# Kernel optimization log

Measured on AMD Instinct MI355X. Metric: run time of the kernel, lower is better.

Reference implementation:

```python
import jax, jax.numpy as jnp
import numpy as np

BLOCKS, LAYERS, KS = 4, 2, 2
DILATIONS = [2 ** i for _ in range(BLOCKS) for i in range(LAYERS)]  # [1,2]*4
B, C_IN, N, T = 16, 2, 2048, 12
RC, DC, SC, EC, OUT = 32, 32, 256, 512, 12
L = BLOCKS * LAYERS
BN_EPS = 1e-5


def setup_inputs() -> dict:
    key = jax.random.key(0)
    ks = jax.random.split(key, 24)
    # raw inputs
    x = jax.random.normal(ks[0], (B, C_IN, N, T), dtype=jnp.float32)
    # two fixed supports: row-normalized random adjacency (dense, as in GraphWaveNet transition matrices)
    A_raw = jax.random.uniform(ks[1], (2, N, N), dtype=jnp.float32)
    A = A_raw / jnp.sum(A_raw, axis=2, keepdims=True)
    nodevec1 = jax.random.normal(ks[2], (N, 10), dtype=jnp.float32)
    nodevec2 = jax.random.normal(ks[3], (10, N), dtype=jnp.float32)
    s = 0.1  # weight scale to keep activations in a sane range
    filter_w = jax.random.normal(ks[4], (L, DC, RC, KS), dtype=jnp.float32) * s
    filter_b = jax.random.normal(ks[5], (L, DC), dtype=jnp.float32) * s
    gate_w = jax.random.normal(ks[6], (L, DC, RC, KS), dtype=jnp.float32) * s
    gate_b = jax.random.normal(ks[7], (L, DC), dtype=jnp.float32) * s
    skip_w = jax.random.normal(ks[8], (L, SC, DC), dtype=jnp.float32) * s
    skip_b = jax.random.normal(ks[9], (L, SC), dtype=jnp.float32) * s
    gcn_w = jax.random.normal(ks[10], (L, RC, 7 * DC), dtype=jnp.float32) * s
    gcn_b = jax.random.normal(ks[11], (L, RC), dtype=jnp.float32) * s
    bn_gamma = 1.0 + 0.1 * jax.random.normal(ks[12], (L, RC), dtype=jnp.float32)
    bn_beta = 0.1 * jax.random.normal(ks[13], (L, RC), dtype=jnp.float32)
    bn_mean = 0.1 * jax.random.normal(ks[14], (L, RC), dtype=jnp.float32)
    bn_var = 1.0 + jax.random.uniform(ks[15], (L, RC), dtype=jnp.float32)
    start_w = jax.random.normal(ks[16], (RC, C_IN), dtype=jnp.float32) * s
    start_b = jax.random.normal(ks[17], (RC,), dtype=jnp.float32) * s
    end1_w = jax.random.normal(ks[18], (EC, SC), dtype=jnp.float32) * s
    end1_b = jax.random.normal(ks[19], (EC,), dtype=jnp.float32) * s
    end2_w = jax.random.normal(ks[20], (OUT, EC), dtype=jnp.float32) * s
    end2_b = jax.random.normal(ks[21], (OUT,), dtype=jnp.float32) * s
    return dict(x=x, A=A, nodevec1=nodevec1, nodevec2=nodevec2,
                filter_w=filter_w, filter_b=filter_b, gate_w=gate_w, gate_b=gate_b,
                skip_w=skip_w, skip_b=skip_b, gcn_w=gcn_w, gcn_b=gcn_b,
                bn_gamma=bn_gamma, bn_beta=bn_beta, bn_mean=bn_mean, bn_var=bn_var,
                start_w=start_w, start_b=start_b, end1_w=end1_w, end1_b=end1_b,
                end2_w=end2_w, end2_b=end2_b)


def _conv1x1(x, w, b):
    # x: [b,c,n,t], w: [o,c] -> [b,o,n,t]
    return jnp.einsum('oc,bcnt->bont', w, x) + b[None, :, None, None]


def _dilated_conv2(x, w, b, d):
    # kernel (1,2) with time dilation d; out length T-d (valid conv)
    xa, xb = x[..., :-d], x[..., d:]
    y = jnp.einsum('oc,bcnt->bont', w[:, :, 0], xa) + jnp.einsum('oc,bcnt->bont', w[:, :, 1], xb)
    return y + b[None, :, None, None]


def _fwd(x, A, nodevec1, nodevec2, filter_w, filter_b, gate_w, gate_b,
         skip_w, skip_b, gcn_w, gcn_b, bn_gamma, bn_beta, bn_mean, bn_var,
         start_w, start_b, end1_w, end1_b, end2_w, end2_b):
    # pad 1 step at the start of time; T becomes 13 == receptive_field
    x = jnp.pad(x, ((0, 0), (0, 0), (0, 0), (1, 0)))
    x = x[:, :2]
    x = _conv1x1(x, start_w, start_b)  # [B,RC,N,13]
    # adaptive adjacency
    adp = jax.nn.softmax(jax.nn.relu(nodevec1 @ nodevec2), axis=1)
    supports = [A[0], A[1], adp]
    skip = None
    for i, d in enumerate(DILATIONS):
        residual = x
        filt = jnp.tanh(_dilated_conv2(residual, filter_w[i], filter_b[i], d))
        gate = jax.nn.sigmoid(_dilated_conv2(residual, gate_w[i], gate_b[i], d))
        x = filt * gate  # [B,DC,N,T-d]
        s = _conv1x1(x, skip_w[i], skip_b[i])  # [B,SC,N,T']
        skip = s if skip is None else s + skip[..., -s.shape[3]:]
        # GCN: order-2 diffusion over 3 supports, concat, 1x1 mix (dropout is identity in eval)
        outs = [x]
        for a in supports:
            x1 = jnp.einsum('bcvt,vw->bcwt', x, a)
            x2 = jnp.einsum('bcvt,vw->bcwt', x1, a)
            outs.extend([x1, x2])
        h = jnp.concatenate(outs, axis=1)  # [B,7*DC,N,T']
        x = _conv1x1(h, gcn_w[i], gcn_b[i])
        x = x + residual[..., -x.shape[3]:]
        # BatchNorm2d in eval mode (running stats)
        inv = bn_gamma[i] / jnp.sqrt(bn_var[i] + BN_EPS)
        x = (x - bn_mean[i][None, :, None, None]) * inv[None, :, None, None] + bn_beta[i][None, :, None, None]
    x = jax.nn.relu(skip)
    x = jax.nn.relu(_conv1x1(x, end1_w, end1_b))
    x = _conv1x1(x, end2_w, end2_b)  # [B,OUT,N,1]
    return x


def reference(x, A, nodevec1, nodevec2, filter_w, filter_b, gate_w, gate_b,
              skip_w, skip_b, gcn_w, gcn_b, bn_gamma, bn_beta, bn_mean, bn_var,
              start_w, start_b, end1_w, end1_b, end2_w, end2_b):
    return _fwd(x, A, nodevec1, nodevec2, filter_w, filter_b, gate_w, gate_b,
                skip_w, skip_b, gcn_w, gcn_b, bn_gamma, bn_beta, bn_mean, bn_var,
                start_w, start_b, end1_w, end1_b, end2_w, end2_b)
```

## Files before the change

kernel.cpp:

```cpp
#include <hip/hip_runtime.h>
#include <math.h>


#define NNODE 2048
#define NLAYER 8
#define SSTR ((size_t)NNODE * NNODE)

typedef unsigned short u16;
typedef unsigned int u32;
typedef __attribute__((ext_vector_type(8))) short bf16x8;
typedef __attribute__((ext_vector_type(4))) float f32x4;

__device__ __forceinline__ u16 f2bf(float f) {
    unsigned u = __builtin_bit_cast(unsigned, f);
    u += 0x7fffu + ((u >> 16) & 1u);
    return (u16)(u >> 16);
}
__device__ __forceinline__ float bf2f(u16 h) {
    unsigned u = ((unsigned)h) << 16;
    return __builtin_bit_cast(float, u);
}
__device__ __forceinline__ float bflo(u32 p) { return __builtin_bit_cast(float, p << 16); }
__device__ __forceinline__ float bfhi(u32 p) { return __builtin_bit_cast(float, p & 0xffff0000u); }
__device__ __forceinline__ u32 pack2(float a, float b) {
    return (u32)f2bf(a) | ((u32)f2bf(b) << 16);
}

__device__ __forceinline__ void gld16(const void* g, void* l) {
    __builtin_amdgcn_global_load_lds(
        (const __attribute__((address_space(1))) unsigned int*)g,
        (__attribute__((address_space(3))) unsigned int*)l, 16, 0, 0);
}

__global__ __launch_bounds__(256) void k_adp_mm(const float* __restrict__ nv1,
                                                const float* __restrict__ nv2,
                                                float* __restrict__ P) {
    int v = blockIdx.y;
    int w = blockIdx.x * 256 + threadIdx.x;
    float acc = 0.f;
#pragma unroll
    for (int k = 0; k < 10; ++k) acc += nv1[v * 10 + k] * nv2[k * NNODE + w];
    P[(size_t)v * NNODE + w] = acc;
}

__global__ __launch_bounds__(256) void k_softmax(float* __restrict__ P) {
    int v = blockIdx.x, tid = threadIdx.x;
    float* row = P + (size_t)v * NNODE;
    float m = 0.f;
    for (int w = tid; w < NNODE; w += 256) m = fmaxf(m, fmaxf(row[w], 0.f));
#pragma unroll
    for (int off = 32; off > 0; off >>= 1) m = fmaxf(m, __shfl_down(m, off));
    __shared__ float redm[4];
    __shared__ float reds[4];
    int wave = tid >> 6, lane = tid & 63;
    if (lane == 0) redm[wave] = m;
    __syncthreads();
    m = fmaxf(fmaxf(redm[0], redm[1]), fmaxf(redm[2], redm[3]));
    float s = 0.f;
    for (int w = tid; w < NNODE; w += 256) s += expf(fmaxf(row[w], 0.f) - m);
#pragma unroll
    for (int off = 32; off > 0; off >>= 1) s += __shfl_down(s, off);
    if (lane == 0) reds[wave] = s;
    __syncthreads();
    s = reds[0] + reds[1] + reds[2] + reds[3];
    float inv = 1.f / s;
    for (int w = tid; w < NNODE; w += 256) row[w] = expf(fmaxf(row[w], 0.f) - m) * inv;
}

__global__ __launch_bounds__(256) void k_transp(const float* __restrict__ A,
                                                const float* __restrict__ adp,
                                                u16* __restrict__ ST,
                                                u16* __restrict__ Sbf) {
    __shared__ float tile[32][33];
    int s = blockIdx.z;
    const float* src = (s < 2) ? (A + (size_t)s * SSTR) : adp;
    int v0 = blockIdx.y * 32, w0 = blockIdx.x * 32;
    int tx = threadIdx.x & 31, ty = threadIdx.x >> 5;
    u16* dst2 = Sbf + (size_t)s * SSTR;
#pragma unroll
    for (int p = 0; p < 4; ++p) {
        float v = src[(size_t)(v0 + ty + p * 8) * NNODE + w0 + tx];
        tile[ty + p * 8][tx] = v;
        dst2[(size_t)(v0 + ty + p * 8) * NNODE + w0 + tx] = f2bf(v);
    }
    __syncthreads();
    u16* dst = ST + (size_t)(2 * s) * SSTR;
#pragma unroll
    for (int p = 0; p < 4; ++p)
        dst[(size_t)(w0 + ty + p * 8) * NNODE + v0 + tx] = f2bf(tile[tx][ty + p * 8]);
}

__global__ __launch_bounds__(256) void k_gemm_mfma(
    const u16* __restrict__ A, int lda, size_t asstr,
    const u16* __restrict__ BT, size_t bsstr,
    u16* __restrict__ C, int ldc, size_t csstr, int sbase) {
    __shared__ u16 Asl[128 * 32];
    __shared__ u16 Bsl[128 * 32];
    const int tid = threadIdx.x;
    const int wave = tid >> 6, lane = tid & 63;
    const int sidx = sbase + blockIdx.z;
    const u16* Ab = A + sidx * asstr + (size_t)blockIdx.y * 128 * lda;
    const u16* Bb = BT + sidx * bsstr + (size_t)blockIdx.x * 128 * NNODE;
    const int tr = tid >> 2;
    const int tc = (tid & 3) * 8;
    char* AslB = (char*)Asl + wave * 1024;
    char* BslB = (char*)Bsl + wave * 1024;
    const int wm = (wave & 1) * 64, wn = (wave >> 1) * 64;
    const int fr = lane & 15;
    const int fk = (lane >> 4) * 8;
    f32x4 acc[4][4];
#pragma unroll
    for (int i = 0; i < 4; ++i)
#pragma unroll
        for (int j = 0; j < 4; ++j) acc[i][j] = (f32x4){0.f, 0.f, 0.f, 0.f};

    for (int k0 = 0; k0 < 2048; k0 += 32) {
        gld16(Ab + (size_t)tr * lda + k0 + tc, AslB);
        gld16(Ab + (size_t)(tr + 64) * lda + k0 + tc, AslB + 4096);
        gld16(Bb + (size_t)tr * NNODE + k0 + tc, BslB);
        gld16(Bb + (size_t)(tr + 64) * NNODE + k0 + tc, BslB + 4096);
        __syncthreads();
        bf16x8 af[4], bf[4];
#pragma unroll
        for (int i = 0; i < 4; ++i)
            af[i] = *(const bf16x8*)&Asl[(wm + i * 16 + fr) * 32 + fk];
#pragma unroll
        for (int j = 0; j < 4; ++j)
            bf[j] = *(const bf16x8*)&Bsl[(wn + j * 16 + fr) * 32 + fk];
#pragma unroll
        for (int i = 0; i < 4; ++i)
#pragma unroll
            for (int j = 0; j < 4; ++j)
                acc[i][j] = __builtin_amdgcn_mfma_f32_16x16x32_bf16(af[i], bf[j], acc[i][j], 0, 0, 0);
        __syncthreads();
    }
    u16* Cb = C + sidx * csstr + (size_t)(blockIdx.y * 128 + wm) * ldc + blockIdx.x * 128 + wn;
    const int orow = (lane >> 4) * 4;
#pragma unroll
    for (int i = 0; i < 4; ++i)
#pragma unroll
        for (int j = 0; j < 4; ++j)
#pragma unroll
            for (int r = 0; r < 4; ++r)
                Cb[(size_t)(i * 16 + orow + r) * ldc + j * 16 + fr] = f2bf(acc[i][j][r]);
}

__global__ __launch_bounds__(256) void k_gemmZ(const u16* __restrict__ Xg,
                                               const u16* __restrict__ ST,
                                               u16* __restrict__ Z, int pass) {
    __shared__ u16 Asl[128 * 32];
    __shared__ u16 Bsl[128 * 32];
    const int tid = threadIdx.x;
    const int wave = tid >> 6, lane = tid & 63;
    const int m0 = blockIdx.x * 128;
    const int sl = blockIdx.y >> 4;
    const int nIn = (blockIdx.y & 15) * 128;
    const int slice = pass * 3 + sl;
    const u16* Ab = Xg + (size_t)m0 * 2048;
    const u16* Bb = ST + (size_t)slice * SSTR + (size_t)nIn * NNODE;
    const int tr = tid >> 2;
    const int tc = (tid & 3) * 8;
    char* AslB = (char*)Asl + wave * 1024;
    char* BslB = (char*)Bsl + wave * 1024;
    const int wm = (wave & 1) * 64, wn = (wave >> 1) * 64;
    const int fr = lane & 15;
    const int fk = (lane >> 4) * 8;
    f32x4 acc[4][4];
#pragma unroll
    for (int i = 0; i < 4; ++i)
#pragma unroll
        for (int j = 0; j < 4; ++j) acc[i][j] = (f32x4){0.f, 0.f, 0.f, 0.f};

    for (int k0 = 0; k0 < 2048; k0 += 32) {
        gld16(Ab + (size_t)tr * 2048 + k0 + tc, AslB);
        gld16(Ab + (size_t)(tr + 64) * 2048 + k0 + tc, AslB + 4096);
        gld16(Bb + (size_t)tr * NNODE + k0 + tc, BslB);
        gld16(Bb + (size_t)(tr + 64) * NNODE + k0 + tc, BslB + 4096);
        __syncthreads();
        bf16x8 af[4], bf[4];
#pragma unroll
        for (int i = 0; i < 4; ++i)
            af[i] = *(const bf16x8*)&Asl[(wm + i * 16 + fr) * 32 + fk];
#pragma unroll
        for (int j = 0; j < 4; ++j)
            bf[j] = *(const bf16x8*)&Bsl[(wn + j * 16 + fr) * 32 + fk];
#pragma unroll
        for (int i = 0; i < 4; ++i)
#pragma unroll
            for (int j = 0; j < 4; ++j)
                acc[i][j] = __builtin_amdgcn_mfma_f32_16x16x32_bf16(af[i], bf[j], acc[i][j], 0, 0, 0);
        __syncthreads();
    }
    u16* Cb = Z + (size_t)(m0 + wm) * 6144 + sl * 2048 + nIn + wn;
    const int orow = (lane >> 4) * 4;
#pragma unroll
    for (int i = 0; i < 4; ++i)
#pragma unroll
        for (int j = 0; j < 4; ++j)
#pragma unroll
            for (int r = 0; r < 4; ++r)
                Cb[(size_t)(i * 16 + orow + r) * 6144 + j * 16 + fr] = f2bf(acc[i][j][r]);
}

__global__ __launch_bounds__(256) void k_start(const float* __restrict__ xin,
                                               const float* __restrict__ sw,
                                               const float* __restrict__ sb,
                                               u16* __restrict__ out, int b0) {
    int n = blockIdx.x * 256 + threadIdx.x;
    int t = blockIdx.y;
    int bl = blockIdx.z;
    int b = b0 + bl;
    float x0 = 0.f, x1 = 0.f;
    if (t > 0) {
        x0 = xin[((size_t)(b * 2 + 0) * NNODE + n) * 12 + (t - 1)];
        x1 = xin[((size_t)(b * 2 + 1) * NNODE + n) * 12 + (t - 1)];
    }
#pragma unroll
    for (int co = 0; co < 32; ++co) {
        float v = sw[co * 2 + 0] * x0 + sw[co * 2 + 1] * x1 + sb[co];
        out[((size_t)(bl * 32 + co) * 13 + t) * NNODE + n] = f2bf(v);
    }
}

__global__ __launch_bounds__(256) void k_gate(const u16* __restrict__ cur,
                                              u16* __restrict__ xg,
                                              u16* __restrict__ nxt,
                                              int T, int Tn, int d,
                                              const float* __restrict__ fw,
                                              const float* __restrict__ fb,
                                              const float* __restrict__ gw,
                                              const float* __restrict__ gb,
                                              const float* __restrict__ gcwl,
                                              const float* __restrict__ gcbl,
                                              int donxt) {
    __shared__ float4 wp[1024];
    __shared__ float w0[32][33];
    int tid = threadIdx.x;
#pragma unroll
    for (int u = 0; u < 4; ++u) {
        int idx = tid + u * 256;
        int ci = idx >> 5, co = idx & 31;
        wp[idx] = make_float4(fw[co * 64 + ci * 2], fw[co * 64 + ci * 2 + 1],
                              gw[co * 64 + ci * 2], gw[co * 64 + ci * 2 + 1]);
        w0[ci][co] = gcwl[co * 224 + ci];
    }
    __syncthreads();
    int n = blockIdx.x * 512 + tid * 2;
    int t = blockIdx.y;
    int bl = blockIdx.z;
    float f0[32], f1[32], g0[32], g1[32];
#pragma unroll
    for (int co = 0; co < 32; ++co) { f0[co] = 0.f; f1[co] = 0.f; g0[co] = 0.f; g1[co] = 0.f; }
    for (int ci = 0; ci < 32; ++ci) {
        size_t ba = ((size_t)(bl * 32 + ci) * T + t) * NNODE + n;
        size_t bb = ((size_t)(bl * 32 + ci) * T + t + d) * NNODE + n;
        u32 ua = *(const u32*)&cur[ba];
        u32 ub = *(const u32*)&cur[bb];
        float xa0 = bflo(ua), xa1 = bfhi(ua);
        float xb0 = bflo(ub), xb1 = bfhi(ub);
#pragma unroll
        for (int co = 0; co < 32; ++co) {
            float4 w = wp[ci * 32 + co];
            f0[co] += w.x * xa0 + w.y * xb0;
            f1[co] += w.x * xa1 + w.y * xb1;
            g0[co] += w.z * xa0 + w.w * xb0;
            g1[co] += w.z * xa1 + w.w * xb1;
        }
    }
#pragma unroll
    for (int co = 0; co < 32; ++co) {
        float fbv = fb[co], gbv = gb[co];
        float a0 = tanhf(f0[co] + fbv) * (1.f / (1.f + expf(-(g0[co] + gbv))));
        float a1 = tanhf(f1[co] + fbv) * (1.f / (1.f + expf(-(g1[co] + gbv))));
        f0[co] = a0; f1[co] = a1;
        size_t o = ((size_t)(bl * 32 + co) * Tn + t) * NNODE + n;
        *(u32*)&xg[o] = pack2(a0, a1);
    }
    if (donxt) {
#pragma unroll
        for (int cop = 0; cop < 32; ++cop) {
            float s0 = gcbl[cop], s1 = s0;
#pragma unroll
            for (int ci = 0; ci < 32; ++ci) {
                float wv = w0[ci][cop];
                s0 += wv * f0[ci];
                s1 += wv * f1[ci];
            }
            size_t o = ((size_t)(bl * 32 + cop) * Tn + t) * NNODE + n;
            *(u32*)&nxt[o] = pack2(s0, s1);
        }
    }
}

__global__ __launch_bounds__(256) void k_skip(const u16* __restrict__ xg,
                                              float* __restrict__ skip, int Tn,
                                              const float* __restrict__ sw,
                                              const float* __restrict__ sb, int b0, int init) {
    __shared__ float wl[256];
    int tid = threadIdx.x;
    int sc0 = blockIdx.y * 8;
    wl[tid] = sw[sc0 * 32 + tid];
    __syncthreads();
    int n = blockIdx.x * 512 + tid * 2;
    int bl = blockIdx.z;
    float a0[8], a1[8];
#pragma unroll
    for (int j = 0; j < 8; ++j) { a0[j] = 0.f; a1[j] = 0.f; }
    for (int ci = 0; ci < 32; ci += 2) {
        u32 p0 = *(const u32*)&xg[((size_t)(bl * 32 + ci + 0) * Tn + (Tn - 1)) * NNODE + n];
        u32 p1 = *(const u32*)&xg[((size_t)(bl * 32 + ci + 1) * Tn + (Tn - 1)) * NNODE + n];
        float v00 = bflo(p0), v01 = bfhi(p0);
        float v10 = bflo(p1), v11 = bfhi(p1);
#pragma unroll
        for (int j = 0; j < 8; ++j) {
            float wA = wl[j * 32 + ci], wB = wl[j * 32 + ci + 1];
            a0[j] += wA * v00 + wB * v10;
            a1[j] += wA * v01 + wB * v11;
        }
    }
    int b = b0 + bl;
#pragma unroll
    for (int j = 0; j < 8; ++j) {
        size_t o = ((size_t)(b * 256) + sc0 + j) * NNODE + n;
        float bsv = sb[sc0 + j];
        if (init) {
            *(float2*)&skip[o] = make_float2(a0[j] + bsv, a1[j] + bsv);
        } else {
            float2 old = *(const float2*)&skip[o];
            *(float2*)&skip[o] = make_float2(old.x + a0[j] + bsv, old.y + a1[j] + bsv);
        }
    }
}

__global__ __launch_bounds__(256) void k_accum(const u16* __restrict__ Z,
                                               int cbase,
                                               const float* __restrict__ gcnw,
                                               u16* __restrict__ outp,
                                               const u16* __restrict__ resid,
                                               int Tn, int d, int finalf,
                                               const float* __restrict__ bng,
                                               const float* __restrict__ bnb,
                                               const float* __restrict__ bnm,
                                               const float* __restrict__ bnv) {
    __shared__ float wl[3][32][32];
    int tid = threadIdx.x;
    for (int u = tid; u < 3072; u += 256) {
        int g = u >> 10, ci = (u >> 5) & 31, co = u & 31;
        wl[g][ci][co] = gcnw[co * 224 + cbase + g * 32 + ci];
    }
    __syncthreads();
    int n = blockIdx.x * 512 + tid * 2;
    int t = blockIdx.y, bl = blockIdx.z;
    float a0[32], a1[32];
#pragma unroll
    for (int co = 0; co < 32; ++co) { a0[co] = 0.f; a1[co] = 0.f; }
    for (int ci = 0; ci < 32; ++ci) {
        size_t m = (size_t)(bl * 32 + ci) * Tn + t;
#pragma unroll
        for (int g = 0; g < 3; ++g) {
            u32 zz = *(const u32*)&Z[m * 6144 + g * 2048 + n];
            float v0 = bflo(zz), v1 = bfhi(zz);
#pragma unroll
            for (int cq = 0; cq < 8; ++cq) {
                float4 w = *(const float4*)&wl[g][ci][cq * 4];
                a0[cq * 4 + 0] += w.x * v0; a1[cq * 4 + 0] += w.x * v1;
                a0[cq * 4 + 1] += w.y * v0; a1[cq * 4 + 1] += w.y * v1;
                a0[cq * 4 + 2] += w.z * v0; a1[cq * 4 + 2] += w.z * v1;
                a0[cq * 4 + 3] += w.w * v0; a1[cq * 4 + 3] += w.w * v1;
            }
        }
    }
#pragma unroll
    for (int co = 0; co < 32; ++co) {
        size_t o = ((size_t)(bl * 32 + co) * Tn + t) * NNODE + n;
        u32 oo = *(const u32*)&outp[o];
        float v0 = bflo(oo) + a0[co];
        float v1 = bfhi(oo) + a1[co];
        if (finalf) {
            size_t ro = ((size_t)(bl * 32 + co) * (Tn + d) + t + d) * NNODE + n;
            u32 rr = *(const u32*)&resid[ro];
            v0 += bflo(rr); v1 += bfhi(rr);
            float inv = bng[co] * rsqrtf(bnv[co] + 1e-5f);
            float mu = bnm[co], be = bnb[co];
            v0 = (v0 - mu) * inv + be;
            v1 = (v1 - mu) * inv + be;
        }
        *(u32*)&outp[o] = pack2(v0, v1);
    }
}

__global__ __launch_bounds__(256) void k_skipT(const float* __restrict__ skip,
                                               u16* __restrict__ skipT) {
    __shared__ float tile[32][33];
    int b = blockIdx.z;
    int n0 = blockIdx.x * 32, c0 = blockIdx.y * 32;
    int tx = threadIdx.x & 31, ty = threadIdx.x >> 5;
#pragma unroll
    for (int p = 0; p < 4; ++p)
        tile[ty + p * 8][tx] = skip[((size_t)b * 256 + c0 + ty + p * 8) * NNODE + n0 + tx];
    __syncthreads();
#pragma unroll
    for (int p = 0; p < 4; ++p)
        skipT[((size_t)b * NNODE + n0 + ty + p * 8) * 256 + c0 + tx] =
            f2bf(fmaxf(tile[tx][ty + p * 8], 0.f));
}

__global__ __launch_bounds__(256) void k_cast(const float* __restrict__ src,
                                              u16* __restrict__ dst) {
    int i = blockIdx.x * 256 + threadIdx.x;
    dst[i] = f2bf(src[i]);
}

__global__ __launch_bounds__(256) void k_end1m(const u16* __restrict__ E1,
                                               const u16* __restrict__ skT,
                                               const float* __restrict__ bias,
                                               u16* __restrict__ h) {
    __shared__ u16 Asl[128 * 32];
    __shared__ u16 Bsl[128 * 32];
    const int tid = threadIdx.x;
    const int wave = tid >> 6, lane = tid & 63;
    const int b = blockIdx.z;
    const int m0 = blockIdx.y * 128;
    const int n0 = blockIdx.x * 128;
    const int tr = tid >> 2;
    const int tc = (tid & 3) * 8;
    char* AslB = (char*)Asl + wave * 1024;
    char* BslB = (char*)Bsl + wave * 1024;
    const int wm = (wave & 1) * 64, wn = (wave >> 1) * 64;
    const int fr = lane & 15;
    const int fk = (lane >> 4) * 8;
    const u16* Ab = E1 + (size_t)m0 * 256;
    const u16* Bb = skT + ((size_t)b * NNODE + n0) * 256;
    f32x4 acc[4][4];
#pragma unroll
    for (int i = 0; i < 4; ++i)
#pragma unroll
        for (int j = 0; j < 4; ++j) acc[i][j] = (f32x4){0.f, 0.f, 0.f, 0.f};
    for (int k0 = 0; k0 < 256; k0 += 32) {
        gld16(Ab + (size_t)tr * 256 + k0 + tc, AslB);
        gld16(Ab + (size_t)(tr + 64) * 256 + k0 + tc, AslB + 4096);
        gld16(Bb + (size_t)tr * 256 + k0 + tc, BslB);
        gld16(Bb + (size_t)(tr + 64) * 256 + k0 + tc, BslB + 4096);
        __syncthreads();
        bf16x8 af[4], bf[4];
#pragma unroll
        for (int i = 0; i < 4; ++i)
            af[i] = *(const bf16x8*)&Asl[(wm + i * 16 + fr) * 32 + fk];
#pragma unroll
        for (int j = 0; j < 4; ++j)
            bf[j] = *(const bf16x8*)&Bsl[(wn + j * 16 + fr) * 32 + fk];
#pragma unroll
        for (int i = 0; i < 4; ++i)
#pragma unroll
            for (int j = 0; j < 4; ++j)
                acc[i][j] = __builtin_amdgcn_mfma_f32_16x16x32_bf16(af[i], bf[j], acc[i][j], 0, 0, 0);
        __syncthreads();
    }
    const int orow = (lane >> 4) * 4;
#pragma unroll
    for (int i = 0; i < 4; ++i)
#pragma unroll
        for (int r = 0; r < 4; ++r) {
            int m = m0 + wm + i * 16 + orow + r;
            float bs = bias[m];
            size_t ob = ((size_t)b * 512 + m) * NNODE + n0 + wn;
#pragma unroll
            for (int j = 0; j < 4; ++j)
                h[ob + j * 16 + fr] = f2bf(fmaxf(acc[i][j][r] + bs, 0.f));
        }
}

__global__ __launch_bounds__(256) void k_end2(const u16* __restrict__ h,
                                              const float* __restrict__ w,
                                              const float* __restrict__ bias,
                                              float* __restrict__ out) {
    __shared__ float wl[12][512];
    int tid = threadIdx.x;
    for (int u = tid; u < 6144; u += 256) wl[u >> 9][u & 511] = w[u];
    __syncthreads();
    int n = blockIdx.x * 256 + tid;
    int b = blockIdx.y;
    float acc[12];
#pragma unroll
    for (int o = 0; o < 12; ++o) acc[o] = 0.f;
#pragma unroll 4
    for (int e = 0; e < 512; ++e) {
        float v = bf2f(h[((size_t)(b * 512) + e) * NNODE + n]);
#pragma unroll
        for (int o = 0; o < 12; ++o) acc[o] += wl[o][e] * v;
    }
#pragma unroll
    for (int o = 0; o < 12; ++o)
        out[((size_t)(b * 12) + o) * NNODE + n] = acc[o] + bias[o];
}

extern "C" void kernel_launch(void* const* d_in, const int* in_sizes, int n_in,
                              void* d_out, int out_size, void* d_ws, size_t ws_size,
                              hipStream_t stream) {
    const float* x_in = (const float*)d_in[0];
    const float* A    = (const float*)d_in[1];
    const float* nv1  = (const float*)d_in[2];
    const float* nv2  = (const float*)d_in[3];
    const float* fw   = (const float*)d_in[4];
    const float* fb   = (const float*)d_in[5];
    const float* gw   = (const float*)d_in[6];
    const float* gb   = (const float*)d_in[7];
    const float* skw  = (const float*)d_in[8];
    const float* skb  = (const float*)d_in[9];
    const float* gcw  = (const float*)d_in[10];
    const float* gcb  = (const float*)d_in[11];
    const float* bng  = (const float*)d_in[12];
    const float* bnb  = (const float*)d_in[13];
    const float* bnm  = (const float*)d_in[14];
    const float* bnv  = (const float*)d_in[15];
    const float* stw  = (const float*)d_in[16];
    const float* stb  = (const float*)d_in[17];
    const float* e1w  = (const float*)d_in[18];
    const float* e1b  = (const float*)d_in[19];
    const float* e2w  = (const float*)d_in[20];
    const float* e2b  = (const float*)d_in[21];
    (void)in_sizes; (void)n_in; (void)out_size;

    const int BL = (ws_size >= 239075328UL) ? 16 : 8;
    const int nch = 16 / BL;
    const size_t bufsz = (size_t)BL * 1703936UL;

    char* base = (char*)d_ws;
    u16*   ST   = (u16*)base;
    float* skip = (float*)(base + 50331648UL);
    u16*   bufA = (u16*)(base + 83886080UL);
    u16*   bufB = (u16*)(base + 83886080UL + bufsz);
    u16*   xg   = (u16*)(base + 83886080UL + 2 * bufsz);
    u16*   Z    = (u16*)(base + 83886080UL + 2 * bufsz + (size_t)BL * 1572864UL);
    float* adp  = (float*)Z;
    u16*   Sbf  = (u16*)bufA;
    u16*   h     = (u16*)(base + 83886080UL);
    u16*   skipT = (u16*)(base + 83886080UL + 33554432UL);
    u16*   E1bf  = (u16*)ST;

    k_adp_mm<<<dim3(8, 2048), 256, 0, stream>>>(nv1, nv2, adp);
    k_softmax<<<2048, 256, 0, stream>>>(adp);
    k_transp<<<dim3(64, 64, 3), 256, 0, stream>>>(A, adp, ST, Sbf);
    k_gemm_mfma<<<dim3(16, 16, 3), 256, 0, stream>>>(
        ST, NNODE, 2 * SSTR, Sbf, SSTR, ST + SSTR, NNODE, 2 * SSTR, 0);

    static const int DIL[NLAYER] = {1, 2, 1, 2, 1, 2, 1, 2};
    for (int ch = 0; ch < nch; ++ch) {
        int b0 = ch * BL;
        k_start<<<dim3(8, 13, BL), 256, 0, stream>>>(x_in, stw, stb, bufA, b0);
        u16* cur = bufA;
        u16* nxt = bufB;
        int T = 13;
        for (int i = 0; i < NLAYER; ++i) {
            int d = DIL[i], Tn = T - d;
            int last = (i == NLAYER - 1);
            k_gate<<<dim3(4, Tn, BL), 256, 0, stream>>>(cur, xg, nxt, T, Tn, d,
                fw + i * 2048, fb + i * 32, gw + i * 2048, gb + i * 32,
                gcw + i * 32 * 224, gcb + i * 32, last ? 0 : 1);
            k_skip<<<dim3(4, 32, BL), 256, 0, stream>>>(xg, skip, Tn,
                skw + i * 256 * 32, skb + i * 256, b0, (i == 0) ? 1 : 0);
            if (last) break;
            int MB = BL * Tn / 4;
            const float* gcwi = gcw + i * 32 * 224;
            for (int p = 0; p < 2; ++p) {
                k_gemmZ<<<dim3(MB, 48), 256, 0, stream>>>(xg, ST, Z, p);
                k_accum<<<dim3(4, Tn, BL), 256, 0, stream>>>(
                    Z, 32 + 96 * p, gcwi, nxt, cur, Tn, d, p,
                    bng + i * 32, bnb + i * 32, bnm + i * 32, bnv + i * 32);
            }
            u16* tmp = cur; cur = nxt; nxt = tmp;
            T = Tn;
        }
    }
    k_cast<<<512, 256, 0, stream>>>(e1w, E1bf);
    k_skipT<<<dim3(64, 8, 16), 256, 0, stream>>>(skip, skipT);
    k_end1m<<<dim3(16, 4, 16), 256, 0, stream>>>(E1bf, skipT, e1b, h);
    k_end2<<<dim3(8, 16), 256, 0, stream>>>(h, e2w, e2b, (float*)d_out);
}
```

Baseline: 3.381 ms.

## Fuse skip conv into gate kernel and use bf16 dot2 for 1x1 convs

Moves the skip 1x1 convolution into the gate kernel, computed only by blocks at the last time step, and removes the separate skip launch. The last layer now runs the gate only for the final time step, since only that output feeds skip. The gate, next-layer and accumulate convolutions now use packed bf16 weights in shared memory with the fdot2 bf16 instruction, halving weight traffic and FMA count. Weights are rounded to bf16 instead of kept in fp32, which costs some accuracy. The last-timestep blocks also carry a serial 256-channel skip loop that may cause load imbalance.

After: 3.547 ms. 1.05x slower.

```diff
diff --git a/kernel.cpp b/kernel.cpp
--- a/kernel.cpp
+++ b/kernel.cpp
@@ -25,6 +25,18 @@
 __device__ __forceinline__ u32 pack2(float a, float b) {
     return (u32)f2bf(a) | ((u32)f2bf(b) << 16);
 }
+
+#if defined(__has_builtin) && __has_builtin(__builtin_amdgcn_fdot2_f32_bf16)
+typedef __attribute__((ext_vector_type(2))) __bf16 bf2v;
+__device__ __forceinline__ float dot2bf(u32 w, u32 x, float acc) {
+    return __builtin_amdgcn_fdot2_f32_bf16(__builtin_bit_cast(bf2v, w),
+                                           __builtin_bit_cast(bf2v, x), acc, false);
+}
+#else
+__device__ __forceinline__ float dot2bf(u32 w, u32 x, float acc) {
+    return acc + bflo(w) * bflo(x) + bfhi(w) * bfhi(x);
+}
+#endif
 
 __device__ __forceinline__ void gld16(const void* g, void* l) {
     __builtin_amdgcn_global_load_lds(
@@ -225,28 +237,44 @@
 __global__ __launch_bounds__(256) void k_gate(const u16* __restrict__ cur,
                                               u16* __restrict__ xg,
                                               u16* __restrict__ nxt,
-                                              int T, int Tn, int d,
+                                              float* __restrict__ skip,
+                                              int T, int Tn, int d, int tbase,
                                               const float* __restrict__ fw,
                                               const float* __restrict__ fb,
                                               const float* __restrict__ gw,
                                               const float* __restrict__ gb,
                                               const float* __restrict__ gcwl,
                                               const float* __restrict__ gcbl,
-                                              int donxt) {
-    __shared__ float4 wp[1024];
-    __shared__ float w0[32][33];
+                                              const float* __restrict__ skw,
+                                              const float* __restrict__ skb,
+                                              int b0, int donxt, int skinit) {
+    __shared__ u32 wpf[1024];
+    __shared__ u32 wpg[1024];
+    __shared__ u32 w0p[512];
+    __shared__ u32 wskp[4096];
     int tid = threadIdx.x;
 #pragma unroll
-    for (int u = 0; u < 4; ++u) {
-        int idx = tid + u * 256;
-        int ci = idx >> 5, co = idx & 31;
-        wp[idx] = make_float4(fw[co * 64 + ci * 2], fw[co * 64 + ci * 2 + 1],
-                              gw[co * 64 + ci * 2], gw[co * 64 + ci * 2 + 1]);
-        w0[ci][co] = gcwl[co * 224 + ci];
+    for (int u0 = 0; u0 < 4; ++u0) {
+        int u = tid + u0 * 256;
+        int ci = u >> 5, co = u & 31;
+        wpf[u] = pack2(fw[co * 64 + ci * 2], fw[co * 64 + ci * 2 + 1]);
+        wpg[u] = pack2(gw[co * 64 + ci * 2], gw[co * 64 + ci * 2 + 1]);
+    }
+#pragma unroll
+    for (int u0 = 0; u0 < 2; ++u0) {
+        int u = tid + u0 * 256;
+        int cip = u >> 5, co = u & 31;
+        w0p[u] = pack2(gcwl[co * 224 + 2 * cip], gcwl[co * 224 + 2 * cip + 1]);
+    }
+#pragma unroll
+    for (int u0 = 0; u0 < 16; ++u0) {
+        int u = tid + u0 * 256;
+        int co = u >> 4, cip = u & 15;
+        wskp[u] = pack2(skw[co * 32 + 2 * cip], skw[co * 32 + 2 * cip + 1]);
     }
     __syncthreads();
     int n = blockIdx.x * 512 + tid * 2;
-    int t = blockIdx.y;
+    int t = blockIdx.y + tbase;
     int bl = blockIdx.z;
     float f0[32], f1[32], g0[32], g1[32];
 #pragma unroll
@@ -256,15 +284,28 @@
         size_t bb = ((size_t)(bl * 32 + ci) * T + t + d) * NNODE + n;
         u32 ua = *(const u32*)&cur[ba];
         u32 ub = *(const u32*)&cur[bb];
-        float xa0 = bflo(ua), xa1 = bfhi(ua);
-        float xb0 = bflo(ub), xb1 = bfhi(ub);
-#pragma unroll
-        for (int co = 0; co < 32; ++co) {
-            float4 w = wp[ci * 32 + co];
-            f0[co] += w.x * xa0 + w.y * xb0;
-            f1[co] += w.x * xa1 + w.y * xb1;
-            g0[co] += w.z * xa0 + w.w * xb0;
-            g1[co] += w.z * xa1 + w.w * xb1;
+        u32 p0 = (ua & 0xffffu) | (ub << 16);
+        u32 p1 = (ua >> 16) | (ub & 0xffff0000u);
+#pragma unroll
+        for (int cq = 0; cq < 8; ++cq) {
+            uint4 wf = *(const uint4*)&wpf[ci * 32 + cq * 4];
+            uint4 wg = *(const uint4*)&wpg[ci * 32 + cq * 4];
+            f0[cq * 4 + 0] = dot2bf(wf.x, p0, f0[cq * 4 + 0]);
+            f1[cq * 4 + 0] = dot2bf(wf.x, p1, f1[cq * 4 + 0]);
+            f0[cq * 4 + 1] = dot2bf(wf.y, p0, f0[cq * 4 + 1]);
+            f1[cq * 4 + 1] = dot2bf(wf.y, p1, f1[cq * 4 + 1]);
+            f0[cq * 4 + 2] = dot2bf(wf.z, p0, f0[cq * 4 + 2]);
+            f1[cq * 4 + 2] = dot2bf(wf.z, p1, f1[cq * 4 + 2]);
+            f0[cq * 4 + 3] = dot2bf(wf.w, p0, f0[cq * 4 + 3]);
+            f1[cq * 4 + 3] = dot2bf(wf.w, p1, f1[cq * 4 + 3]);
+            g0[cq * 4 + 0] = dot2bf(wg.x, p0, g0[cq * 4 + 0]);
+            g1[cq * 4 + 0] = dot2bf(wg.x, p1, g1[cq * 4 + 0]);
+            g0[cq * 4 + 1] = dot2bf(wg.y, p0, g0[cq * 4 + 1]);
+            g1[cq * 4 + 1] = dot2bf(wg.y, p1, g1[cq * 4 + 1]);
+            g0[cq * 4 + 2] = dot2bf(wg.z, p0, g0[cq * 4 + 2]);
+            g1[cq * 4 + 2] = dot2bf(wg.z, p1, g1[cq * 4 + 2]);
+            g0[cq * 4 + 3] = dot2bf(wg.w, p0, g0[cq * 4 + 3]);
+            g1[cq * 4 + 3] = dot2bf(wg.w, p1, g1[cq * 4 + 3]);
         }
     }
 #pragma unroll
@@ -273,61 +314,62 @@
         float a0 = tanhf(f0[co] + fbv) * (1.f / (1.f + expf(-(g0[co] + gbv))));
         float a1 = tanhf(f1[co] + fbv) * (1.f / (1.f + expf(-(g1[co] + gbv))));
         f0[co] = a0; f1[co] = a1;
-        size_t o = ((size_t)(bl * 32 + co) * Tn + t) * NNODE + n;
-        *(u32*)&xg[o] = pack2(a0, a1);
+        if (donxt) {
+            size_t o = ((size_t)(bl * 32 + co) * Tn + t) * NNODE + n;
+            *(u32*)&xg[o] = pack2(a0, a1);
+        }
+    }
+    u32 fp0[16], fp1[16];
+#pragma unroll
+    for (int cip = 0; cip < 16; ++cip) {
+        fp0[cip] = pack2(f0[2 * cip], f0[2 * cip + 1]);
+        fp1[cip] = pack2(f1[2 * cip], f1[2 * cip + 1]);
     }
     if (donxt) {
 #pragma unroll
         for (int cop = 0; cop < 32; ++cop) {
             float s0 = gcbl[cop], s1 = s0;
 #pragma unroll
-            for (int ci = 0; ci < 32; ++ci) {
-                float wv = w0[ci][cop];
-                s0 += wv * f0[ci];
-                s1 += wv * f1[ci];
+            for (int c4 = 0; c4 < 4; ++c4) {
+                uint4 w = *(const uint4*)&w0p[(c4 * 4) * 32 + cop];
+                s0 = dot2bf(w0p[(c4 * 4 + 0) * 32 + cop], fp0[c4 * 4 + 0], s0);
+                s1 = dot2bf(w0p[(c4 * 4 + 0) * 32 + cop], fp1[c4 * 4 + 0], s1);
+                s0 = dot2bf(w0p[(c4 * 4 + 1) * 32 + cop], fp0[c4 * 4 + 1], s0);
+                s1 = dot2bf(w0p[(c4 * 4 + 1) * 32 + cop], fp1[c4 * 4 + 1], s1);
+                s0 = dot2bf(w0p[(c4 * 4 + 2) * 32 + cop], fp0[c4 * 4 + 2], s0);
+                s1 = dot2bf(w0p[(c4 * 4 + 2) * 32 + cop], fp1[c4 * 4 + 2], s1);
+                s0 = dot2bf(w0p[(c4 * 4 + 3) * 32 + cop], fp0[c4 * 4 + 3], s0);
+                s1 = dot2bf(w0p[(c4 * 4 + 3) * 32 + cop], fp1[c4 * 4 + 3], s1);
+                (void)w;
             }
             size_t o = ((size_t)(bl * 32 + cop) * Tn + t) * NNODE + n;
             *(u32*)&nxt[o] = pack2(s0, s1);
         }
     }
-}
-
-__global__ __launch_bounds__(256) void k_skip(const u16* __restrict__ xg,
-                                              float* __restrict__ skip, int Tn,
-                                              const float* __restrict__ sw,
-                                              const float* __restrict__ sb, int b0, int init) {
-    __shared__ float wl[256];
-    int tid = threadIdx.x;
-    int sc0 = blockIdx.y * 8;
-    wl[tid] = sw[sc0 * 32 + tid];
-    __syncthreads();
-    int n = blockIdx.x * 512 + tid * 2;
-    int bl = blockIdx.z;
-    float a0[8], a1[8];
-#pragma unroll
-    for (int j = 0; j < 8; ++j) { a0[j] = 0.f; a1[j] = 0.f; }
-    for (int ci = 0; ci < 32; ci += 2) {
-        u32 p0 = *(const u32*)&xg[((size_t)(bl * 32 + ci + 0) * Tn + (Tn - 1)) * NNODE + n];
-        u32 p1 = *(const u32*)&xg[((size_t)(bl * 32 + ci + 1) * Tn + (Tn - 1)) * NNODE + n];
-        float v00 = bflo(p0), v01 = bfhi(p0);
-        float v10 = bflo(p1), v11 = bfhi(p1);
-#pragma unroll
-        for (int j = 0; j < 8; ++j) {
-            float wA = wl[j * 32 + ci], wB = wl[j * 32 + ci + 1];
-            a0[j] += wA * v00 + wB * v10;
-            a1[j] += wA * v01 + wB * v11;
-        }
-    }
-    int b = b0 + bl;
-#pragma unroll
-    for (int j = 0; j < 8; ++j) {
-        size_t o = ((size_t)(b * 256) + sc0 + j) * NNODE + n;
-        float bsv = sb[sc0 + j];
-        if (init) {
-            *(float2*)&skip[o] = make_float2(a0[j] + bsv, a1[j] + bsv);
-        } else {
-            float2 old = *(const float2*)&skip[o];
-            *(float2*)&skip[o] = make_float2(old.x + a0[j] + bsv, old.y + a1[j] + bsv);
+    if (t == Tn - 1) {
+        int b = b0 + bl;
+        for (int cop = 0; cop < 256; ++cop) {
+            float a0 = 0.f, a1 = 0.f;
+#pragma unroll
+            for (int c4 = 0; c4 < 4; ++c4) {
+                uint4 w = *(const uint4*)&wskp[cop * 16 + c4 * 4];
+                a0 = dot2bf(w.x, fp0[c4 * 4 + 0], a0);
+                a1 = dot2bf(w.x, fp1[c4 * 4 + 0], a1);
+                a0 = dot2bf(w.y, fp0[c4 * 4 + 1], a0);
+                a1 = dot2bf(w.y, fp1[c4 * 4 + 1], a1);
+                a0 = dot2bf(w.z, fp0[c4 * 4 + 2], a0);
+                a1 = dot2bf(w.z, fp1[c4 * 4 + 2], a1);
+                a0 = dot2bf(w.w, fp0[c4 * 4 + 3], a0);
+                a1 = dot2bf(w.w, fp1[c4 * 4 + 3], a1);
+            }
+            size_t o = ((size_t)(b * 256) + cop) * NNODE + n;
+            float bs = skb[cop];
+            if (skinit) {
+                *(float2*)&skip[o] = make_float2(a0 + bs, a1 + bs);
+            } else {
+                float2 old = *(const float2*)&skip[o];
+                *(float2*)&skip[o] = make_float2(old.x + a0 + bs, old.y + a1 + bs);
+            }
         }
     }
 }
@@ -342,11 +384,12 @@
                                                const float* __restrict__ bnb,
                                                const float* __restrict__ bnm,
                                                const float* __restrict__ bnv) {
-    __shared__ float wl[3][32][32];
+    __shared__ u32 wp3[3][16][32];
     int tid = threadIdx.x;
-    for (int u = tid; u < 3072; u += 256) {
-        int g = u >> 10, ci = (u >> 5) & 31, co = u & 31;
-        wl[g][ci][co] = gcnw[co * 224 + cbase + g * 32 + ci];
+    for (int u = tid; u < 1536; u += 256) {
+        int g = u >> 9, cip = (u >> 5) & 15, co = u & 31;
+        wp3[g][cip][co] = pack2(gcnw[co * 224 + cbase + g * 32 + 2 * cip],
+                                gcnw[co * 224 + cbase + g * 32 + 2 * cip + 1]);
     }
     __syncthreads();
     int n = blockIdx.x * 512 + tid * 2;
@@ -354,19 +397,26 @@
     float a0[32], a1[32];
 #pragma unroll
     for (int co = 0; co < 32; ++co) { a0[co] = 0.f; a1[co] = 0.f; }
-    for (int ci = 0; ci < 32; ++ci) {
-        size_t m = (size_t)(bl * 32 + ci) * Tn + t;
+    for (int cip = 0; cip < 16; ++cip) {
+        size_t m0r = (size_t)(bl * 32 + 2 * cip) * Tn + t;
+        size_t m1r = m0r + Tn;
 #pragma unroll
         for (int g = 0; g < 3; ++g) {
-            u32 zz = *(const u32*)&Z[m * 6144 + g * 2048 + n];
-            float v0 = bflo(zz), v1 = bfhi(zz);
+            u32 z0 = *(const u32*)&Z[m0r * 6144 + g * 2048 + n];
+            u32 z1 = *(const u32*)&Z[m1r * 6144 + g * 2048 + n];
+            u32 pk0 = (z0 & 0xffffu) | (z1 << 16);
+            u32 pk1 = (z0 >> 16) | (z1 & 0xffff0000u);
 #pragma unroll
             for (int cq = 0; cq < 8; ++cq) {
-                float4 w = *(const float4*)&wl[g][ci][cq * 4];
-                a0[cq * 4 + 0] += w.x * v0; a1[cq * 4 + 0] += w.x * v1;
-                a0[cq * 4 + 1] += w.y * v0; a1[cq * 4 + 1] += w.y * v1;
-                a0[cq * 4 + 2] += w.z * v0; a1[cq * 4 + 2] += w.z * v1;
-                a0[cq * 4 + 3] += w.w * v0; a1[cq * 4 + 3] += w.w * v1;
+                uint4 w = *(const uint4*)&wp3[g][cip][cq * 4];
+                a0[cq * 4 + 0] = dot2bf(w.x, pk0, a0[cq * 4 + 0]);
+                a1[cq * 4 + 0] = dot2bf(w.x, pk1, a1[cq * 4 + 0]);
+                a0[cq * 4 + 1] = dot2bf(w.y, pk0, a0[cq * 4 + 1]);
+                a1[cq * 4 + 1] = dot2bf(w.y, pk1, a1[cq * 4 + 1]);
+                a0[cq * 4 + 2] = dot2bf(w.z, pk0, a0[cq * 4 + 2]);
+                a1[cq * 4 + 2] = dot2bf(w.z, pk1, a1[cq * 4 + 2]);
+                a0[cq * 4 + 3] = dot2bf(w.w, pk0, a0[cq * 4 + 3]);
+                a1[cq * 4 + 3] = dot2bf(w.w, pk1, a1[cq * 4 + 3]);
             }
         }
     }
@@ -554,12 +604,19 @@
         for (int i = 0; i < NLAYER; ++i) {
             int d = DIL[i], Tn = T - d;
             int last = (i == NLAYER - 1);
-            k_gate<<<dim3(4, Tn, BL), 256, 0, stream>>>(cur, xg, nxt, T, Tn, d,
+            if (last) {
+                k_gate<<<dim3(4, 1, BL), 256, 0, stream>>>(cur, xg, nxt, skip,
+                    T, Tn, d, Tn - 1,
+                    fw + i * 2048, fb + i * 32, gw + i * 2048, gb + i * 32,
+                    gcw + i * 32 * 224, gcb + i * 32,
+                    skw + i * 256 * 32, skb + i * 256, b0, 0, 0);
+                break;
+            }
+            k_gate<<<dim3(4, Tn, BL), 256, 0, stream>>>(cur, xg, nxt, skip,
+                T, Tn, d, 0,
                 fw + i * 2048, fb + i * 32, gw + i * 2048, gb + i * 32,
-                gcw + i * 32 * 224, gcb + i * 32, last ? 0 : 1);
-            k_skip<<<dim3(4, 32, BL), 256, 0, stream>>>(xg, skip, Tn,
-                skw + i * 256 * 32, skb + i * 256, b0, (i == 0) ? 1 : 0);
-            if (last) break;
+                gcw + i * 32 * 224, gcb + i * 32,
+                skw + i * 256 * 32, skb + i * 256, b0, 1, (i == 0) ? 1 : 0);
             int MB = BL * Tn / 4;
             const float* gcwi = gcw + i * 32 * 224;
             for (int p = 0; p < 2; ++p) {
```
